# Performance work log

Hardware: AMD Instinct MI355X
Metric: run time of the kernel (lower is better)

Reference implementation:

```python
import jax, jax.numpy as jnp
import numpy as np

EMBED = 1024
HEADS = 16
HEAD_DIM = EMBED // HEADS


def setup_inputs() -> dict:
    key = jax.random.key(0)
    ks = jax.random.split(key, 7)
    B, S = 4, 2048
    q = jax.random.normal(ks[0], (B, S, EMBED), dtype=jnp.float32)
    k = jax.random.normal(ks[1], (B, S, EMBED), dtype=jnp.float32)
    v = jax.random.normal(ks[2], (B, S, EMBED), dtype=jnp.float32)
    # causal mask, broadcast over heads: [B, 1, S, S]
    mask = jnp.broadcast_to(jnp.tril(jnp.ones((S, S), dtype=jnp.int32))[None, None], (B, 1, S, S))
    scale = 1.0 / np.sqrt(EMBED)
    w_q = jax.random.normal(ks[3], (EMBED, EMBED), dtype=jnp.float32) * scale
    w_k = jax.random.normal(ks[4], (EMBED, EMBED), dtype=jnp.float32) * scale
    w_v = jax.random.normal(ks[5], (EMBED, EMBED), dtype=jnp.float32) * scale
    w_o = jax.random.normal(ks[6], (EMBED, EMBED), dtype=jnp.float32) * scale
    return {"q": q, "k": k, "v": v, "mask": mask,
            "w_q": w_q, "w_k": w_k, "w_v": w_v, "w_o": w_o}


def reference(q, k, v, mask, w_q, w_k, w_v, w_o):
    B, S, _ = q.shape
    # Linear projections (torch Linear: x @ W^T), split into heads: [B,H,S,D]
    def proj(x, w):
        return (x @ w.T).reshape(B, -1, HEADS, HEAD_DIM).transpose(0, 2, 1, 3)
    qh, kh, vh = proj(q, w_q), proj(k, w_k), proj(v, w_v)
    scores = jnp.einsum('bhqd,bhkd->bhqk', qh, kh) / jnp.sqrt(jnp.float32(HEAD_DIM))
    scores = jnp.where(mask == 0, jnp.float32(-1e9), scores)
    attn = jax.nn.softmax(scores, axis=-1)
    # dropout is identity in eval/reference mode
    x = jnp.einsum('bhqk,bhkd->bhqd', attn, vh)  # [B,H,S,D]
    x = x.transpose(0, 2, 1, 3).reshape(B, S, HEADS * HEAD_DIM)
    return x @ w_o.T
```

## Files before the change

### kernel.cpp

```cpp
#include <hip/hip_runtime.h>

typedef unsigned short u16;
typedef __attribute__((ext_vector_type(8))) short v8s;
typedef __attribute__((ext_vector_type(4))) float v4f;

#define S_LEN  2048
#define NHEADS 16
#define DHEAD  64
#define EMB    1024

#if __has_builtin(__builtin_amdgcn_exp2f)
#define EXP2F __builtin_amdgcn_exp2f
#else
#define EXP2F exp2f
#endif

__device__ __forceinline__ u16 f32_bf16(float f) {
  union { float f; unsigned u; } x; x.f = f;
  unsigned r = x.u + 0x7fffu + ((x.u >> 16) & 1u);
  return (u16)(r >> 16);
}

__device__ __forceinline__ void async16(const void* g, void* l) {
  __builtin_amdgcn_global_load_lds(
      (const __attribute__((address_space(1))) unsigned int*)g,
      (__attribute__((address_space(3))) unsigned int*)l, 16, 0, 0);
}

__global__ __launch_bounds__(256) void cvt_all(
    const float4* __restrict__ s0, const float4* __restrict__ s1,
    const float4* __restrict__ s2, const float4* __restrict__ s3,
    const float4* __restrict__ s4, const float4* __restrict__ s5,
    const float4* __restrict__ s6,
    ushort4* __restrict__ d0, ushort4* __restrict__ d1,
    ushort4* __restrict__ d2, ushort4* __restrict__ d3,
    ushort4* __restrict__ d4, ushort4* __restrict__ d5,
    ushort4* __restrict__ d6, int nbig, int nsmall) {
  const int y = blockIdx.y;
  const float4* s; ushort4* d;
  switch (y) {
    case 0: s = s0; d = d0; break;  case 1: s = s1; d = d1; break;
    case 2: s = s2; d = d2; break;  case 3: s = s3; d = d3; break;
    case 4: s = s4; d = d4; break;  case 5: s = s5; d = d5; break;
    default: s = s6; d = d6; break;
  }
  const int n4 = (y < 3) ? nbig : nsmall;
  for (int i = blockIdx.x * 256 + threadIdx.x; i < n4; i += gridDim.x * 256) {
    const float4 v = s[i];
    ushort4 o;
    o.x = f32_bf16(v.x); o.y = f32_bf16(v.y);
    o.z = f32_bf16(v.z); o.w = f32_bf16(v.w);
    d[i] = o;
  }
}

template <int MODE>
__global__ __launch_bounds__(512, 2) void gemm2ph(
    const u16* __restrict__ A, const u16* __restrict__ W0,
    const u16* __restrict__ W1, const u16* __restrict__ W2,
    u16* __restrict__ Cq, u16* __restrict__ Ck, u16* __restrict__ Cv,
    float* __restrict__ Cf, int mtiles) {
  const int K = 1024;
  const int NKT = 16;
  __shared__ __align__(16) u16 lA[2][128 * 64];
  __shared__ __align__(16) u16 lB[2][128 * 64];
  const int t = threadIdx.x;
  const int lane = t & 63, wv = t >> 6;
  const int wm = wv >> 2, wn = wv & 3;
  const int qr = lane >> 4, cl = lane & 15;

  const int nwg = gridDim.x;
  const int sid = (blockIdx.x & 7) * (nwg >> 3) + (blockIdx.x >> 3);
  const int bm = sid % mtiles, bn = sid / mtiles;
  const int m0 = bm << 7, n0 = bn << 7;
  const int sec = (MODE == 0) ? (m0 >> 13) : 0;
  const u16* W =
      (MODE == 0) ? ((sec == 0) ? W0 : (sec == 1) ? W1 : W2) : W0;

  v4f acc[4][2];
#pragma unroll
  for (int i = 0; i < 4; ++i)
#pragma unroll
    for (int j = 0; j < 2; ++j) acc[i][j] = (v4f){0.f, 0.f, 0.f, 0.f};

  const int srow = t >> 3;
  const int sw = ((t & 7) ^ (srow & 7)) << 3;
  const u16* aS[2];
  const u16* bS[2];
#pragma unroll
  for (int u = 0; u < 2; ++u) {
    aS[u] = A + (size_t)(m0 + srow + u * 64) * K + sw;
    bS[u] = W + (size_t)(n0 + srow + u * 64) * K + sw;
  }

#pragma unroll
  for (int u = 0; u < 2; ++u) async16(aS[u], &lA[0][(t + (u << 9)) << 3]);
#pragma unroll
  for (int u = 0; u < 2; ++u) async16(bS[u], &lB[0][(t + (u << 9)) << 3]);
  __syncthreads();

  for (int kt = 0; kt < NKT; ++kt) {
    const int cur = kt & 1;
    if (kt + 1 < NKT) {
      const int off = (kt + 1) << 6;
#pragma unroll
      for (int u = 0; u < 2; ++u)
        async16(aS[u] + off, &lA[1 - cur][(t + (u << 9)) << 3]);
#pragma unroll
      for (int u = 0; u < 2; ++u)
        async16(bS[u] + off, &lB[1 - cur][(t + (u << 9)) << 3]);
    }
    v8s a[4][2], b[2][2];
#pragma unroll
    for (int mf = 0; mf < 4; ++mf)
#pragma unroll
      for (int kh = 0; kh < 2; ++kh) {
        const int R = wm * 64 + mf * 16 + cl;
        a[mf][kh] =
            *(const v8s*)&lA[cur][R * 64 + ((((kh << 2) + qr) ^ (R & 7)) << 3)];
      }
#pragma unroll
    for (int nf = 0; nf < 2; ++nf)
#pragma unroll
      for (int kh = 0; kh < 2; ++kh) {
        const int R = wn * 32 + nf * 16 + cl;
        b[nf][kh] =
            *(const v8s*)&lB[cur][R * 64 + ((((kh << 2) + qr) ^ (R & 7)) << 3)];
      }
    __builtin_amdgcn_s_setprio(1);
#pragma unroll
    for (int kh = 0; kh < 2; ++kh)
#pragma unroll
      for (int mf = 0; mf < 4; ++mf)
#pragma unroll
        for (int nf = 0; nf < 2; ++nf)
          acc[mf][nf] = __builtin_amdgcn_mfma_f32_16x16x32_bf16(
              a[mf][kh], b[nf][kh], acc[mf][nf], 0, 0, 0);
    __builtin_amdgcn_s_setprio(0);
    __syncthreads();
  }

  if constexpr (MODE == 0) {
    u16* C = (sec == 0) ? Cq : (sec == 1) ? Ck : Cv;
#pragma unroll
    for (int mf = 0; mf < 4; ++mf)
#pragma unroll
      for (int nf = 0; nf < 2; ++nf)
#pragma unroll
        for (int r = 0; r < 4; ++r) {
          const int mloc = (m0 & 8191) + wm * 64 + mf * 16 + qr * 4 + r;
          const int n = n0 + wn * 32 + nf * 16 + cl;
          const int bb = mloc >> 11, s = mloc & (S_LEN - 1);
          const int h = n >> 6, d = n & (DHEAD - 1);
          const size_t idx =
              (sec < 2) ? (((size_t)bb * NHEADS + h) * S_LEN + s) * DHEAD + d
                        : (((size_t)bb * NHEADS + h) * DHEAD + d) * S_LEN + s;
          C[idx] = f32_bf16(acc[mf][nf][r]);
        }
  } else {
#pragma unroll
    for (int mf = 0; mf < 4; ++mf)
#pragma unroll
      for (int nf = 0; nf < 2; ++nf)
#pragma unroll
        for (int r = 0; r < 4; ++r) {
          const int m = m0 + wm * 64 + mf * 16 + qr * 4 + r;
          const int n = n0 + wn * 32 + nf * 16 + cl;
          Cf[(size_t)m * 1024 + n] = acc[mf][nf][r];
        }
  }
}

__global__ __launch_bounds__(256, 2) void attn_causal(
    const u16* __restrict__ Qp, const u16* __restrict__ Kp,
    const u16* __restrict__ VpT, u16* __restrict__ Out) {
  __shared__ __align__(16) u16 lK[2][2][64 * 64];
  __shared__ __align__(16) u16 lV[2][2][64 * 64];
  __shared__ __align__(16) u16 pb[4][32 * 64];
  const int t = threadIdx.x;
  const int lane = t & 63, w = t >> 6;
  const int qr = lane >> 4, cl = lane & 15;
  const int id = blockIdx.x;
  const int col = (id & 7) + ((id >> 6) << 3);
  const int pair = (id >> 3) & 7;
  const int h = col & 15, b = col >> 4;
  const size_t bh = ((size_t)b * NHEADS + h) * S_LEN * DHEAD;
  const u16* Qb = Qp + bh;
  const u16* Kb = Kp + bh;
  const u16* Vb = VpT + bh;

  v8s vone;
#pragma unroll
  for (int j = 0; j < 8; ++j) vone[j] = (short)0x3F80;
  const float SC = 0.125f * 1.4426950408889634f;

#define STAGE_T(TILE, GP, SL)                                                 \
  do {                                                                        \
    const int kn_ = (TILE) << 6;                                              \
    _Pragma("unroll") for (int i_ = 0; i_ < 2; ++i_) {                        \
      const int c_ = t + (i_ << 8);                                           \
      const int krow_ = c_ >> 3, kdc_ = (c_ & 7) ^ (krow_ & 7);               \
      async16(Kb + (size_t)(kn_ + krow_) * DHEAD + kdc_ * 8,                  \
              &lK[GP][SL][(w * 64 + (i_ << 8)) * 8]);                         \
      const int vd_ = c_ >> 3, vkc_ = (c_ & 7) ^ (vd_ & 7);                   \
      async16(Vb + (size_t)vd_ * S_LEN + kn_ + vkc_ * 8,                      \
              &lV[GP][SL][(w * 64 + (i_ << 8)) * 8]);                         \
    }                                                                         \
  } while (0)

  for (int phase = 0; phase < 2; ++phase) {
    const int qt = phase == 0 ? (15 - pair) : pair;
    const int q0 = qt << 7;
    const int wr0 = q0 + w * 32;

    v8s aq[2][2];
#pragma unroll
    for (int mf = 0; mf < 2; ++mf)
#pragma unroll
      for (int kf = 0; kf < 2; ++kf)
        aq[mf][kf] = *(const v8s*)(Qb + (size_t)(wr0 + mf * 16 + cl) * DHEAD +
                                   kf * 32 + qr * 8);

    v4f o[2][4], lac[2];
#pragma unroll
    for (int mf = 0; mf < 2; ++mf) {
      lac[mf] = (v4f){0.f, 0.f, 0.f, 0.f};
#pragma unroll
      for (int nf = 0; nf < 4; ++nf) o[mf][nf] = (v4f){0.f, 0.f, 0.f, 0.f};
    }

    const int ngrp = qt + 1;
    __syncthreads();
    STAGE_T(0, 0, 0);
    STAGE_T(1, 0, 1);

    for (int g = 0; g < ngrp; ++g) {
      const int gp = g & 1;
      __syncthreads();
      if (g + 1 < ngrp) {
        STAGE_T(2 * g + 2, 1 - gp, 0);
        STAGE_T(2 * g + 3, 1 - gp, 1);
      }
#pragma unroll
      for (int sl = 0; sl < 2; ++sl) {
        const int kt = 2 * g + sl;
        const int k0 = kt << 6;
        if (k0 > wr0 + 31) continue;
        const u16* lKc = &lK[gp][sl][0];
        const u16* lVc = &lV[gp][sl][0];

        v4f sacc[2][4];
#pragma unroll
        for (int mf = 0; mf < 2; ++mf)
#pragma unroll
          for (int ni = 0; ni < 4; ++ni) sacc[mf][ni] = (v4f){0.f, 0.f, 0.f, 0.f};
#pragma unroll
        for (int kf = 0; kf < 2; ++kf)
#pragma unroll
          for (int ni = 0; ni < 4; ++ni) {
            const v8s bk = *(const v8s*)&lKc[((ni * 16 + cl) * 8 +
                                             (((kf << 2) + qr) ^ (cl & 7))) * 8];
            sacc[0][ni] = __builtin_amdgcn_mfma_f32_16x16x32_bf16(
                aq[0][kf], bk, sacc[0][ni], 0, 0, 0);
            sacc[1][ni] = __builtin_amdgcn_mfma_f32_16x16x32_bf16(
                aq[1][kf], bk, sacc[1][ni], 0, 0, 0);
          }

#pragma unroll
        for (int mf = 0; mf < 2; ++mf) {
          const int rowb0 = wr0 + mf * 16;
          if (k0 + 63 <= rowb0) {
#pragma unroll
            for (int ni = 0; ni < 4; ++ni) {
              const int kc = ni * 2 + (cl >> 3);
#pragma unroll
              for (int r = 0; r < 4; ++r) {
                const float e = EXP2F(sacc[mf][ni][r] * SC);
                pb[w][((kc * 32 + mf * 16 + r * 4 + qr) << 3) + (cl & 7)] =
                    (u16)(__float_as_uint(e) >> 16);
              }
            }
          } else {
            const int rowb = rowb0 + qr * 4;
#pragma unroll
            for (int ni = 0; ni < 4; ++ni) {
              const int colk = k0 + ni * 16 + cl;
              const int kc = ni * 2 + (cl >> 3);
#pragma unroll
              for (int r = 0; r < 4; ++r) {
                float e = EXP2F(sacc[mf][ni][r] * SC);
                if (colk > rowb + r) e = 0.f;
                pb[w][((kc * 32 + mf * 16 + r * 4 + qr) << 3) + (cl & 7)] =
                    (u16)(__float_as_uint(e) >> 16);
              }
            }
          }
        }

#pragma unroll
        for (int kf = 0; kf < 2; ++kf) {
          const int kc = (kf << 2) + qr;
          const int sig0 = ((cl & 3) << 2) + (cl >> 2);
          const v8s ap0 = *(const v8s*)&pb[w][((kc * 32 + sig0) << 3)];
          const v8s ap1 = *(const v8s*)&pb[w][((kc * 32 + 16 + sig0) << 3)];
          lac[0] = __builtin_amdgcn_mfma_f32_16x16x32_bf16(ap0, vone, lac[0], 0, 0, 0);
          lac[1] = __builtin_amdgcn_mfma_f32_16x16x32_bf16(ap1, vone, lac[1], 0, 0, 0);
#pragma unroll
          for (int nf = 0; nf < 4; ++nf) {
            const v8s bv = *(const v8s*)&lVc[((nf * 16 + cl) * 8 +
                                             (kc ^ (cl & 7))) * 8];
            o[0][nf] = __builtin_amdgcn_mfma_f32_16x16x32_bf16(ap0, bv, o[0][nf], 0, 0, 0);
            o[1][nf] = __builtin_amdgcn_mfma_f32_16x16x32_bf16(ap1, bv, o[1][nf], 0, 0, 0);
          }
        }
      }
    }

#pragma unroll
    for (int mf = 0; mf < 2; ++mf) {
      float inv[4];
#pragma unroll
      for (int r = 0; r < 4; ++r) inv[r] = 1.0f / lac[mf][r];
#pragma unroll
      for (int nf = 0; nf < 4; ++nf)
#pragma unroll
        for (int r = 0; r < 4; ++r) {
          const int row = wr0 + mf * 16 + qr * 4 + r;
          const int colo = h * DHEAD + nf * 16 + cl;
          Out[((size_t)b * S_LEN + row) * EMB + colo] = f32_bf16(o[mf][nf][r] * inv[r]);
        }
    }
  }
#undef STAGE_T
}

extern "C" void kernel_launch(void* const* d_in, const int* in_sizes, int n_in,
                              void* d_out, int out_size, void* d_ws, size_t ws_size,
                              hipStream_t stream) {
  (void)in_sizes; (void)n_in; (void)out_size; (void)ws_size;
  const float* q  = (const float*)d_in[0];
  const float* k  = (const float*)d_in[1];
  const float* v  = (const float*)d_in[2];
  const float* wq = (const float*)d_in[4];
  const float* wk = (const float*)d_in[5];
  const float* wv = (const float*)d_in[6];
  const float* wo = (const float*)d_in[7];
  float* out = (float*)d_out;

  const size_t MT = (size_t)4 * S_LEN * EMB;
  const size_t WT = (size_t)EMB * EMB;
  u16* p = (u16*)d_ws;
  u16* xq = p; p += MT;
  u16* xk = p; p += MT;
  u16* xv = p; p += MT;
  u16* wqb = p; p += WT;
  u16* wkb = p; p += WT;
  u16* wvb = p; p += WT;
  u16* wob = p; p += WT;
  u16* Qp = p; p += MT;
  u16* Kp = p; p += MT;
  u16* Vp = p; p += MT;
  u16* Ao = xq;

  const dim3 blk(256);
  hipLaunchKernelGGL(cvt_all, dim3(512, 7), blk, 0, stream,
                     (const float4*)q, (const float4*)k, (const float4*)v,
                     (const float4*)wq, (const float4*)wk, (const float4*)wv,
                     (const float4*)wo,
                     (ushort4*)xq, (ushort4*)xk, (ushort4*)xv,
                     (ushort4*)wqb, (ushort4*)wkb, (ushort4*)wvb, (ushort4*)wob,
                     (int)(MT / 4), (int)(WT / 4));
  hipLaunchKernelGGL((gemm2ph<0>), dim3(1536), dim3(512), 0, stream,
                     xq, wqb, wkb, wvb, Qp, Kp, Vp, (float*)nullptr, 192);
  hipLaunchKernelGGL(attn_causal, dim3(512), blk, 0, stream, Qp, Kp, Vp, Ao);
  hipLaunchKernelGGL((gemm2ph<1>), dim3(512), dim3(512), 0, stream,
                     Ao, wob, (const u16*)nullptr, (const u16*)nullptr,
                     (u16*)nullptr, (u16*)nullptr, (u16*)nullptr, out, 64);
}
```

Measured before the change: 340.7 us.

## Use triple-buffered K=32 LDS pipeline with vmcnt waits in projection GEMMs

The projection GEMMs move from a double-buffered K=64 tile loop to a three-stage ring of K=32 tiles. Each stage is prefetched two tiles ahead, and the per-iteration __syncthreads is replaced by an explicit s_waitcnt vmcnt plus a single barrier. LDS offsets are precomputed once under a new swizzle layout. The aim is to keep more global-to-LDS loads in flight so the MFMAs stall less on memory, at the cost of twice as many iterations and barriers and reliance on hand-managed wait counts.

```diff
diff --git a/kernel.cpp b/kernel.cpp
--- a/kernel.cpp
+++ b/kernel.cpp
@@ -26,6 +26,8 @@
       (const __attribute__((address_space(1))) unsigned int*)g,
       (__attribute__((address_space(3))) unsigned int*)l, 16, 0, 0);
 }
+
+#define FENCE() asm volatile("" ::: "memory")
 
 __global__ __launch_bounds__(256) void cvt_all(
     const float4* __restrict__ s0, const float4* __restrict__ s1,
@@ -55,15 +57,15 @@
 }
 
 template <int MODE>
-__global__ __launch_bounds__(512, 2) void gemm2ph(
+__global__ __launch_bounds__(512, 2) void gemm3p(
     const u16* __restrict__ A, const u16* __restrict__ W0,
     const u16* __restrict__ W1, const u16* __restrict__ W2,
     u16* __restrict__ Cq, u16* __restrict__ Ck, u16* __restrict__ Cv,
     float* __restrict__ Cf, int mtiles) {
   const int K = 1024;
-  const int NKT = 16;
-  __shared__ __align__(16) u16 lA[2][128 * 64];
-  __shared__ __align__(16) u16 lB[2][128 * 64];
+  const int NKT = 32;
+  __shared__ __align__(16) u16 lA[3][4096];
+  __shared__ __align__(16) u16 lB[3][4096];
   const int t = threadIdx.x;
   const int lane = t & 63, wv = t >> 6;
   const int wm = wv >> 2, wn = wv & 3;
@@ -83,62 +85,69 @@
 #pragma unroll
     for (int j = 0; j < 2; ++j) acc[i][j] = (v4f){0.f, 0.f, 0.f, 0.f};
 
-  const int srow = t >> 3;
-  const int sw = ((t & 7) ^ (srow & 7)) << 3;
-  const u16* aS[2];
-  const u16* bS[2];
-#pragma unroll
-  for (int u = 0; u < 2; ++u) {
-    aS[u] = A + (size_t)(m0 + srow + u * 64) * K + sw;
-    bS[u] = W + (size_t)(n0 + srow + u * 64) * K + sw;
-  }
-
-#pragma unroll
-  for (int u = 0; u < 2; ++u) async16(aS[u], &lA[0][(t + (u << 9)) << 3]);
-#pragma unroll
-  for (int u = 0; u < 2; ++u) async16(bS[u], &lB[0][(t + (u << 9)) << 3]);
-  __syncthreads();
-
+  const int Lt = t >> 3;
+  const int pt = (t & 7) ^ (Lt & 7);
+  const int rh = (pt >> 2) << 6;
+  const int kc8 = (pt & 3) << 3;
+  const u16* aS = A + (size_t)(m0 + Lt + rh) * K + kc8;
+  const u16* bS = W + (size_t)(n0 + Lt + rh) * K + kc8;
+
+  int aOff[4], bOff[2];
+#pragma unroll
+  for (int f = 0; f < 4; ++f) {
+    const int R = wm * 64 + f * 16 + cl;
+    aOff[f] = (R & 63) * 64 + (((((R >> 6) << 2) | qr) ^ (cl & 7)) << 3);
+  }
+#pragma unroll
+  for (int nf = 0; nf < 2; ++nf) {
+    const int R = wn * 32 + nf * 16 + cl;
+    bOff[nf] = (R & 63) * 64 + (((((R >> 6) << 2) | qr) ^ (cl & 7)) << 3);
+  }
+
+#define STG(TILE, BUF)                                                        \
+  do {                                                                        \
+    const int ko_ = (TILE) << 5;                                              \
+    async16(aS + ko_, &lA[BUF][t * 8]);                                       \
+    async16(bS + ko_, &lB[BUF][t * 8]);                                       \
+  } while (0)
+
+#define BODY(CUR)                                                             \
+  do {                                                                        \
+    v8s a_[4], b_[2];                                                         \
+    _Pragma("unroll") for (int mf = 0; mf < 4; ++mf)                          \
+        a_[mf] = *(const v8s*)&lA[CUR][aOff[mf]];                             \
+    _Pragma("unroll") for (int nf = 0; nf < 2; ++nf)                          \
+        b_[nf] = *(const v8s*)&lB[CUR][bOff[nf]];                             \
+    __builtin_amdgcn_s_setprio(1);                                            \
+    _Pragma("unroll") for (int mf = 0; mf < 4; ++mf)                          \
+        _Pragma("unroll") for (int nf = 0; nf < 2; ++nf)                      \
+            acc[mf][nf] = __builtin_amdgcn_mfma_f32_16x16x32_bf16(            \
+                a_[mf], b_[nf], acc[mf][nf], 0, 0, 0);                        \
+    __builtin_amdgcn_s_setprio(0);                                            \
+  } while (0)
+
+  STG(0, 0);
+  STG(1, 1);
+  FENCE();
+
+  int cur = 0, stg = 2;
   for (int kt = 0; kt < NKT; ++kt) {
-    const int cur = kt & 1;
-    if (kt + 1 < NKT) {
-      const int off = (kt + 1) << 6;
-#pragma unroll
-      for (int u = 0; u < 2; ++u)
-        async16(aS[u] + off, &lA[1 - cur][(t + (u << 9)) << 3]);
-#pragma unroll
-      for (int u = 0; u < 2; ++u)
-        async16(bS[u] + off, &lB[1 - cur][(t + (u << 9)) << 3]);
+    if (kt < NKT - 1) {
+      asm volatile("s_waitcnt vmcnt(2)" ::: "memory");
+    } else {
+      asm volatile("s_waitcnt vmcnt(0)" ::: "memory");
     }
-    v8s a[4][2], b[2][2];
-#pragma unroll
-    for (int mf = 0; mf < 4; ++mf)
-#pragma unroll
-      for (int kh = 0; kh < 2; ++kh) {
-        const int R = wm * 64 + mf * 16 + cl;
-        a[mf][kh] =
-            *(const v8s*)&lA[cur][R * 64 + ((((kh << 2) + qr) ^ (R & 7)) << 3)];
-      }
-#pragma unroll
-    for (int nf = 0; nf < 2; ++nf)
-#pragma unroll
-      for (int kh = 0; kh < 2; ++kh) {
-        const int R = wn * 32 + nf * 16 + cl;
-        b[nf][kh] =
-            *(const v8s*)&lB[cur][R * 64 + ((((kh << 2) + qr) ^ (R & 7)) << 3)];
-      }
-    __builtin_amdgcn_s_setprio(1);
-#pragma unroll
-    for (int kh = 0; kh < 2; ++kh)
-#pragma unroll
-      for (int mf = 0; mf < 4; ++mf)
-#pragma unroll
-        for (int nf = 0; nf < 2; ++nf)
-          acc[mf][nf] = __builtin_amdgcn_mfma_f32_16x16x32_bf16(
-              a[mf][kh], b[nf][kh], acc[mf][nf], 0, 0, 0);
-    __builtin_amdgcn_s_setprio(0);
-    __syncthreads();
-  }
+    FENCE();
+    __builtin_amdgcn_s_barrier();
+    FENCE();
+    if (kt + 2 < NKT) STG(kt + 2, stg);
+    BODY(cur);
+    cur = (cur == 2) ? 0 : cur + 1;
+    stg = (stg == 2) ? 0 : stg + 1;
+  }
+
+#undef STG
+#undef BODY
 
   if constexpr (MODE == 0) {
     u16* C = (sec == 0) ? Cq : (sec == 1) ? Ck : Cv;
@@ -370,10 +379,10 @@
                      (ushort4*)xq, (ushort4*)xk, (ushort4*)xv,
                      (ushort4*)wqb, (ushort4*)wkb, (ushort4*)wvb, (ushort4*)wob,
                      (int)(MT / 4), (int)(WT / 4));
-  hipLaunchKernelGGL((gemm2ph<0>), dim3(1536), dim3(512), 0, stream,
+  hipLaunchKernelGGL((gemm3p<0>), dim3(1536), dim3(512), 0, stream,
                      xq, wqb, wkb, wvb, Qp, Kp, Vp, (float*)nullptr, 192);
   hipLaunchKernelGGL(attn_causal, dim3(512), blk, 0, stream, Qp, Kp, Vp, Ao);
-  hipLaunchKernelGGL((gemm2ph<1>), dim3(512), dim3(512), 0, stream,
+  hipLaunchKernelGGL((gemm3p<1>), dim3(512), dim3(512), 0, stream,
                      Ao, wob, (const u16*)nullptr, (const u16*)nullptr,
                      (u16*)nullptr, (u16*)nullptr, (u16*)nullptr, out, 64);
 }
```

Result: slower. 353.0 us (+3.6%).

## Run both causal query tiles concurrently in one 512-thread attention block

Applied to the files above, without the earlier changes.

The attention kernel now processes the two paired query tiles (15-pair and pair) at the same time with 8 waves instead of sequentially with 4. The shared K/V tiles are staged once per key tile and reused by both halves, and staging changes from 2-tile groups to single-tile double buffering. This removes the second pass's redundant K/V loads and the serial phase, at the cost of larger blocks, more LDS for the probability buffers, and idle waves for the short tile once its causal range ends.

```diff
diff --git a/kernel.cpp b/kernel.cpp
--- a/kernel.cpp
+++ b/kernel.cpp
@@ -171,12 +171,12 @@
   }
 }
 
-__global__ __launch_bounds__(256, 2) void attn_causal(
+__global__ __launch_bounds__(512, 2) void attn_causal(
     const u16* __restrict__ Qp, const u16* __restrict__ Kp,
     const u16* __restrict__ VpT, u16* __restrict__ Out) {
-  __shared__ __align__(16) u16 lK[2][2][64 * 64];
-  __shared__ __align__(16) u16 lV[2][2][64 * 64];
-  __shared__ __align__(16) u16 pb[4][32 * 64];
+  __shared__ __align__(16) u16 lK[2][64 * 64];
+  __shared__ __align__(16) u16 lV[2][64 * 64];
+  __shared__ __align__(16) u16 pb[8][32 * 64];
   const int t = threadIdx.x;
   const int lane = t & 63, w = t >> 6;
   const int qr = lane >> 4, cl = lane & 15;
@@ -194,142 +194,123 @@
   for (int j = 0; j < 8; ++j) vone[j] = (short)0x3F80;
   const float SC = 0.125f * 1.4426950408889634f;
 
-#define STAGE_T(TILE, GP, SL)                                                 \
+#define STAGE_T(TILE, SL)                                                     \
   do {                                                                        \
     const int kn_ = (TILE) << 6;                                              \
-    _Pragma("unroll") for (int i_ = 0; i_ < 2; ++i_) {                        \
-      const int c_ = t + (i_ << 8);                                           \
-      const int krow_ = c_ >> 3, kdc_ = (c_ & 7) ^ (krow_ & 7);               \
-      async16(Kb + (size_t)(kn_ + krow_) * DHEAD + kdc_ * 8,                  \
-              &lK[GP][SL][(w * 64 + (i_ << 8)) * 8]);                         \
-      const int vd_ = c_ >> 3, vkc_ = (c_ & 7) ^ (vd_ & 7);                   \
-      async16(Vb + (size_t)vd_ * S_LEN + kn_ + vkc_ * 8,                      \
-              &lV[GP][SL][(w * 64 + (i_ << 8)) * 8]);                         \
-    }                                                                         \
+    const int r_ = t >> 3, c_ = (t & 7) ^ (r_ & 7);                           \
+    async16(Kb + (size_t)(kn_ + r_) * DHEAD + c_ * 8, &lK[SL][t * 8]);        \
+    async16(Vb + (size_t)r_ * S_LEN + kn_ + c_ * 8, &lV[SL][t * 8]);          \
   } while (0)
 
-  for (int phase = 0; phase < 2; ++phase) {
-    const int qt = phase == 0 ? (15 - pair) : pair;
-    const int q0 = qt << 7;
-    const int wr0 = q0 + w * 32;
-
-    v8s aq[2][2];
+  const int qt = (w < 4) ? (15 - pair) : pair;
+  const int q0 = qt << 7;
+  const int wr0 = q0 + (w & 3) * 32;
+  const int nkt = 32 - 2 * pair;
+
+  v8s aq[2][2];
+#pragma unroll
+  for (int mf = 0; mf < 2; ++mf)
+#pragma unroll
+    for (int kf = 0; kf < 2; ++kf)
+      aq[mf][kf] = *(const v8s*)(Qb + (size_t)(wr0 + mf * 16 + cl) * DHEAD +
+                                 kf * 32 + qr * 8);
+
+  v4f o[2][4], lac[2];
+#pragma unroll
+  for (int mf = 0; mf < 2; ++mf) {
+    lac[mf] = (v4f){0.f, 0.f, 0.f, 0.f};
+#pragma unroll
+    for (int nf = 0; nf < 4; ++nf) o[mf][nf] = (v4f){0.f, 0.f, 0.f, 0.f};
+  }
+
+  STAGE_T(0, 0);
+
+  for (int kt = 0; kt < nkt; ++kt) {
+    const int k0 = kt << 6;
+    const int cb = kt & 1;
+    __syncthreads();
+    if (kt + 1 < nkt) STAGE_T(kt + 1, 1 - cb);
+    if (k0 > wr0 + 31) continue;
+
+    v4f sacc[2][4];
 #pragma unroll
     for (int mf = 0; mf < 2; ++mf)
 #pragma unroll
-      for (int kf = 0; kf < 2; ++kf)
-        aq[mf][kf] = *(const v8s*)(Qb + (size_t)(wr0 + mf * 16 + cl) * DHEAD +
-                                   kf * 32 + qr * 8);
-
-    v4f o[2][4], lac[2];
+      for (int ni = 0; ni < 4; ++ni) sacc[mf][ni] = (v4f){0.f, 0.f, 0.f, 0.f};
+#pragma unroll
+    for (int kf = 0; kf < 2; ++kf)
+#pragma unroll
+      for (int ni = 0; ni < 4; ++ni) {
+        const v8s bk = *(const v8s*)&lK[cb][((ni * 16 + cl) * 8 +
+                                            (((kf << 2) + qr) ^ (cl & 7))) * 8];
+        sacc[0][ni] = __builtin_amdgcn_mfma_f32_16x16x32_bf16(aq[0][kf], bk,
+                                                              sacc[0][ni], 0, 0, 0);
+        sacc[1][ni] = __builtin_amdgcn_mfma_f32_16x16x32_bf16(aq[1][kf], bk,
+                                                              sacc[1][ni], 0, 0, 0);
+      }
+
 #pragma unroll
     for (int mf = 0; mf < 2; ++mf) {
-      lac[mf] = (v4f){0.f, 0.f, 0.f, 0.f};
-#pragma unroll
-      for (int nf = 0; nf < 4; ++nf) o[mf][nf] = (v4f){0.f, 0.f, 0.f, 0.f};
-    }
-
-    const int ngrp = qt + 1;
-    __syncthreads();
-    STAGE_T(0, 0, 0);
-    STAGE_T(1, 0, 1);
-
-    for (int g = 0; g < ngrp; ++g) {
-      const int gp = g & 1;
-      __syncthreads();
-      if (g + 1 < ngrp) {
-        STAGE_T(2 * g + 2, 1 - gp, 0);
-        STAGE_T(2 * g + 3, 1 - gp, 1);
-      }
-#pragma unroll
-      for (int sl = 0; sl < 2; ++sl) {
-        const int kt = 2 * g + sl;
-        const int k0 = kt << 6;
-        if (k0 > wr0 + 31) continue;
-        const u16* lKc = &lK[gp][sl][0];
-        const u16* lVc = &lV[gp][sl][0];
-
-        v4f sacc[2][4];
-#pragma unroll
-        for (int mf = 0; mf < 2; ++mf)
-#pragma unroll
-          for (int ni = 0; ni < 4; ++ni) sacc[mf][ni] = (v4f){0.f, 0.f, 0.f, 0.f};
-#pragma unroll
-        for (int kf = 0; kf < 2; ++kf)
-#pragma unroll
-          for (int ni = 0; ni < 4; ++ni) {
-            const v8s bk = *(const v8s*)&lKc[((ni * 16 + cl) * 8 +
-                                             (((kf << 2) + qr) ^ (cl & 7))) * 8];
-            sacc[0][ni] = __builtin_amdgcn_mfma_f32_16x16x32_bf16(
-                aq[0][kf], bk, sacc[0][ni], 0, 0, 0);
-            sacc[1][ni] = __builtin_amdgcn_mfma_f32_16x16x32_bf16(
-                aq[1][kf], bk, sacc[1][ni], 0, 0, 0);
-          }
-
-#pragma unroll
-        for (int mf = 0; mf < 2; ++mf) {
-          const int rowb0 = wr0 + mf * 16;
-          if (k0 + 63 <= rowb0) {
-#pragma unroll
-            for (int ni = 0; ni < 4; ++ni) {
-              const int kc = ni * 2 + (cl >> 3);
-#pragma unroll
-              for (int r = 0; r < 4; ++r) {
-                const float e = EXP2F(sacc[mf][ni][r] * SC);
-                pb[w][((kc * 32 + mf * 16 + r * 4 + qr) << 3) + (cl & 7)] =
-                    (u16)(__float_as_uint(e) >> 16);
-              }
-            }
-          } else {
-            const int rowb = rowb0 + qr * 4;
-#pragma unroll
-            for (int ni = 0; ni < 4; ++ni) {
-              const int colk = k0 + ni * 16 + cl;
-              const int kc = ni * 2 + (cl >> 3);
-#pragma unroll
-              for (int r = 0; r < 4; ++r) {
-                float e = EXP2F(sacc[mf][ni][r] * SC);
-                if (colk > rowb + r) e = 0.f;
-                pb[w][((kc * 32 + mf * 16 + r * 4 + qr) << 3) + (cl & 7)] =
-                    (u16)(__float_as_uint(e) >> 16);
-              }
-            }
+      const int rowb0 = wr0 + mf * 16;
+      if (k0 + 63 <= rowb0) {
+#pragma unroll
+        for (int ni = 0; ni < 4; ++ni) {
+          const int kc = ni * 2 + (cl >> 3);
+#pragma unroll
+          for (int r = 0; r < 4; ++r) {
+            const float e = EXP2F(sacc[mf][ni][r] * SC);
+            pb[w][((kc * 32 + mf * 16 + r * 4 + qr) << 3) + (cl & 7)] =
+                (u16)(__float_as_uint(e) >> 16);
           }
         }
-
-#pragma unroll
-        for (int kf = 0; kf < 2; ++kf) {
-          const int kc = (kf << 2) + qr;
-          const int sig0 = ((cl & 3) << 2) + (cl >> 2);
-          const v8s ap0 = *(const v8s*)&pb[w][((kc * 32 + sig0) << 3)];
-          const v8s ap1 = *(const v8s*)&pb[w][((kc * 32 + 16 + sig0) << 3)];
-          lac[0] = __builtin_amdgcn_mfma_f32_16x16x32_bf16(ap0, vone, lac[0], 0, 0, 0);
-          lac[1] = __builtin_amdgcn_mfma_f32_16x16x32_bf16(ap1, vone, lac[1], 0, 0, 0);
-#pragma unroll
-          for (int nf = 0; nf < 4; ++nf) {
-            const v8s bv = *(const v8s*)&lVc[((nf * 16 + cl) * 8 +
-                                             (kc ^ (cl & 7))) * 8];
-            o[0][nf] = __builtin_amdgcn_mfma_f32_16x16x32_bf16(ap0, bv, o[0][nf], 0, 0, 0);
-            o[1][nf] = __builtin_amdgcn_mfma_f32_16x16x32_bf16(ap1, bv, o[1][nf], 0, 0, 0);
+      } else {
+        const int rowb = rowb0 + qr * 4;
+#pragma unroll
+        for (int ni = 0; ni < 4; ++ni) {
+          const int colk = k0 + ni * 16 + cl;
+          const int kc = ni * 2 + (cl >> 3);
+#pragma unroll
+          for (int r = 0; r < 4; ++r) {
+            float e = EXP2F(sacc[mf][ni][r] * SC);
+            if (colk > rowb + r) e = 0.f;
+            pb[w][((kc * 32 + mf * 16 + r * 4 + qr) << 3) + (cl & 7)] =
+                (u16)(__float_as_uint(e) >> 16);
           }
         }
       }
     }
 
 #pragma unroll
-    for (int mf = 0; mf < 2; ++mf) {
-      float inv[4];
-#pragma unroll
-      for (int r = 0; r < 4; ++r) inv[r] = 1.0f / lac[mf][r];
-#pragma unroll
-      for (int nf = 0; nf < 4; ++nf)
-#pragma unroll
-        for (int r = 0; r < 4; ++r) {
-          const int row = wr0 + mf * 16 + qr * 4 + r;
-          const int colo = h * DHEAD + nf * 16 + cl;
-          Out[((size_t)b * S_LEN + row) * EMB + colo] = f32_bf16(o[mf][nf][r] * inv[r]);
-        }
+    for (int kf = 0; kf < 2; ++kf) {
+      const int kc = (kf << 2) + qr;
+      const int sig0 = ((cl & 3) << 2) + (cl >> 2);
+      const v8s ap0 = *(const v8s*)&pb[w][((kc * 32 + sig0) << 3)];
+      const v8s ap1 = *(const v8s*)&pb[w][((kc * 32 + 16 + sig0) << 3)];
+      lac[0] = __builtin_amdgcn_mfma_f32_16x16x32_bf16(ap0, vone, lac[0], 0, 0, 0);
+      lac[1] = __builtin_amdgcn_mfma_f32_16x16x32_bf16(ap1, vone, lac[1], 0, 0, 0);
+#pragma unroll
+      for (int nf = 0; nf < 4; ++nf) {
+        const v8s bv = *(const v8s*)&lV[cb][((nf * 16 + cl) * 8 +
+                                            (kc ^ (cl & 7))) * 8];
+        o[0][nf] = __builtin_amdgcn_mfma_f32_16x16x32_bf16(ap0, bv, o[0][nf], 0, 0, 0);
+        o[1][nf] = __builtin_amdgcn_mfma_f32_16x16x32_bf16(ap1, bv, o[1][nf], 0, 0, 0);
+      }
     }
+  }
+
+#pragma unroll
+  for (int mf = 0; mf < 2; ++mf) {
+    float inv[4];
+#pragma unroll
+    for (int r = 0; r < 4; ++r) inv[r] = 1.0f / lac[mf][r];
+#pragma unroll
+    for (int nf = 0; nf < 4; ++nf)
+#pragma unroll
+      for (int r = 0; r < 4; ++r) {
+        const int row = wr0 + mf * 16 + qr * 4 + r;
+        const int colo = h * DHEAD + nf * 16 + cl;
+        Out[((size_t)b * S_LEN + row) * EMB + colo] = f32_bf16(o[mf][nf][r] * inv[r]);
+      }
   }
 #undef STAGE_T
 }
@@ -372,7 +353,8 @@
                      (int)(MT / 4), (int)(WT / 4));
   hipLaunchKernelGGL((gemm2ph<0>), dim3(1536), dim3(512), 0, stream,
                      xq, wqb, wkb, wvb, Qp, Kp, Vp, (float*)nullptr, 192);
-  hipLaunchKernelGGL(attn_causal, dim3(512), blk, 0, stream, Qp, Kp, Vp, Ao);
+  hipLaunchKernelGGL(attn_causal, dim3(512), dim3(512), 0, stream,
+                     Qp, Kp, Vp, Ao);
   hipLaunchKernelGGL((gemm2ph<1>), dim3(512), dim3(512), 0, stream,
                      Ao, wob, (const u16*)nullptr, (const u16*)nullptr,
                      (u16*)nullptr, (u16*)nullptr, (u16*)nullptr, out, 64);
```

After: 375.6 us. 10.2% more time.

## Fuse fp32-to-bf16 activation conversion into the QKV projection GEMM

Applied to the files above, without the earlier changes.

The standalone conversion of the q/k/v activations to bf16 is removed. The QKV GEMM now loads fp32 rows directly into registers, converts them, and writes the bf16 values into swizzled LDS for the next k-tile after the MFMA block, replacing the async global-to-LDS path for the A operand. This drops a full write and re-read of the three bf16 activation buffers. In exchange, the GEMM reads twice as many bytes for A, uses more registers for the fp32 staging values, and does the conversion ALU work inside the main loop.

```diff
diff --git a/kernel.cpp b/kernel.cpp
--- a/kernel.cpp
+++ b/kernel.cpp
@@ -27,24 +27,17 @@
       (__attribute__((address_space(3))) unsigned int*)l, 16, 0, 0);
 }
 
-__global__ __launch_bounds__(256) void cvt_all(
+__global__ __launch_bounds__(256) void cvt_w(
     const float4* __restrict__ s0, const float4* __restrict__ s1,
     const float4* __restrict__ s2, const float4* __restrict__ s3,
-    const float4* __restrict__ s4, const float4* __restrict__ s5,
-    const float4* __restrict__ s6,
     ushort4* __restrict__ d0, ushort4* __restrict__ d1,
-    ushort4* __restrict__ d2, ushort4* __restrict__ d3,
-    ushort4* __restrict__ d4, ushort4* __restrict__ d5,
-    ushort4* __restrict__ d6, int nbig, int nsmall) {
+    ushort4* __restrict__ d2, ushort4* __restrict__ d3, int n4) {
   const int y = blockIdx.y;
   const float4* s; ushort4* d;
   switch (y) {
     case 0: s = s0; d = d0; break;  case 1: s = s1; d = d1; break;
-    case 2: s = s2; d = d2; break;  case 3: s = s3; d = d3; break;
-    case 4: s = s4; d = d4; break;  case 5: s = s5; d = d5; break;
-    default: s = s6; d = d6; break;
-  }
-  const int n4 = (y < 3) ? nbig : nsmall;
+    case 2: s = s2; d = d2; break;  default: s = s3; d = d3; break;
+  }
   for (int i = blockIdx.x * 256 + threadIdx.x; i < n4; i += gridDim.x * 256) {
     const float4 v = s[i];
     ushort4 o;
@@ -56,8 +49,11 @@
 
 template <int MODE>
 __global__ __launch_bounds__(512, 2) void gemm2ph(
-    const u16* __restrict__ A, const u16* __restrict__ W0,
-    const u16* __restrict__ W1, const u16* __restrict__ W2,
+    const float* __restrict__ F0, const float* __restrict__ F1,
+    const float* __restrict__ F2,
+    const u16* __restrict__ Abf,
+    const u16* __restrict__ W0, const u16* __restrict__ W1,
+    const u16* __restrict__ W2,
     u16* __restrict__ Cq, u16* __restrict__ Ck, u16* __restrict__ Cv,
     float* __restrict__ Cf, int mtiles) {
   const int K = 1024;
@@ -84,28 +80,67 @@
     for (int j = 0; j < 2; ++j) acc[i][j] = (v4f){0.f, 0.f, 0.f, 0.f};
 
   const int srow = t >> 3;
-  const int sw = ((t & 7) ^ (srow & 7)) << 3;
+  const int swe = ((t & 7) ^ (srow & 7)) << 3;
+
+  const float* fS[2];
   const u16* aS[2];
   const u16* bS[2];
-#pragma unroll
-  for (int u = 0; u < 2; ++u) {
-    aS[u] = A + (size_t)(m0 + srow + u * 64) * K + sw;
-    bS[u] = W + (size_t)(n0 + srow + u * 64) * K + sw;
-  }
-
-#pragma unroll
-  for (int u = 0; u < 2; ++u) async16(aS[u], &lA[0][(t + (u << 9)) << 3]);
+  if constexpr (MODE == 0) {
+    const int mloc = m0 & 8191;
+    const float* Fs = (sec == 0) ? F0 : (sec == 1) ? F1 : F2;
+#pragma unroll
+    for (int u = 0; u < 2; ++u)
+      fS[u] = Fs + (size_t)(mloc + srow + u * 64) * K + swe;
+  } else {
+#pragma unroll
+    for (int u = 0; u < 2; ++u)
+      aS[u] = Abf + (size_t)(m0 + srow + u * 64) * K + swe;
+  }
+#pragma unroll
+  for (int u = 0; u < 2; ++u)
+    bS[u] = W + (size_t)(n0 + srow + u * 64) * K + swe;
+
+#define CVT_WRITE(U, BUF, LO, HI)                                             \
+  do {                                                                        \
+    v8s pk_;                                                                  \
+    pk_[0] = (short)f32_bf16((LO).x); pk_[1] = (short)f32_bf16((LO).y);       \
+    pk_[2] = (short)f32_bf16((LO).z); pk_[3] = (short)f32_bf16((LO).w);       \
+    pk_[4] = (short)f32_bf16((HI).x); pk_[5] = (short)f32_bf16((HI).y);       \
+    pk_[6] = (short)f32_bf16((HI).z); pk_[7] = (short)f32_bf16((HI).w);       \
+    *(v8s*)&lA[BUF][(t + ((U) << 9)) << 3] = pk_;                             \
+  } while (0)
+
+  if constexpr (MODE == 0) {
+#pragma unroll
+    for (int u = 0; u < 2; ++u) {
+      const float4 lo = *(const float4*)(fS[u]);
+      const float4 hi = *(const float4*)(fS[u] + 4);
+      CVT_WRITE(u, 0, lo, hi);
+    }
+  } else {
+#pragma unroll
+    for (int u = 0; u < 2; ++u) async16(aS[u], &lA[0][(t + (u << 9)) << 3]);
+  }
 #pragma unroll
   for (int u = 0; u < 2; ++u) async16(bS[u], &lB[0][(t + (u << 9)) << 3]);
   __syncthreads();
 
   for (int kt = 0; kt < NKT; ++kt) {
     const int cur = kt & 1;
+    float4 fa0[2], fa1[2];
     if (kt + 1 < NKT) {
       const int off = (kt + 1) << 6;
-#pragma unroll
-      for (int u = 0; u < 2; ++u)
-        async16(aS[u] + off, &lA[1 - cur][(t + (u << 9)) << 3]);
+      if constexpr (MODE == 0) {
+#pragma unroll
+        for (int u = 0; u < 2; ++u) {
+          fa0[u] = *(const float4*)(fS[u] + off);
+          fa1[u] = *(const float4*)(fS[u] + off + 4);
+        }
+      } else {
+#pragma unroll
+        for (int u = 0; u < 2; ++u)
+          async16(aS[u] + off, &lA[1 - cur][(t + (u << 9)) << 3]);
+      }
 #pragma unroll
       for (int u = 0; u < 2; ++u)
         async16(bS[u] + off, &lB[1 - cur][(t + (u << 9)) << 3]);
@@ -137,8 +172,15 @@
           acc[mf][nf] = __builtin_amdgcn_mfma_f32_16x16x32_bf16(
               a[mf][kh], b[nf][kh], acc[mf][nf], 0, 0, 0);
     __builtin_amdgcn_s_setprio(0);
+    if constexpr (MODE == 0) {
+      if (kt + 1 < NKT) {
+#pragma unroll
+        for (int u = 0; u < 2; ++u) CVT_WRITE(u, 1 - cur, fa0[u], fa1[u]);
+      }
+    }
     __syncthreads();
   }
+#undef CVT_WRITE
 
   if constexpr (MODE == 0) {
     u16* C = (sec == 0) ? Cq : (sec == 1) ? Ck : Cv;
@@ -350,9 +392,6 @@
   const size_t MT = (size_t)4 * S_LEN * EMB;
   const size_t WT = (size_t)EMB * EMB;
   u16* p = (u16*)d_ws;
-  u16* xq = p; p += MT;
-  u16* xk = p; p += MT;
-  u16* xv = p; p += MT;
   u16* wqb = p; p += WT;
   u16* wkb = p; p += WT;
   u16* wvb = p; p += WT;
@@ -360,20 +399,21 @@
   u16* Qp = p; p += MT;
   u16* Kp = p; p += MT;
   u16* Vp = p; p += MT;
-  u16* Ao = xq;
-
-  const dim3 blk(256);
-  hipLaunchKernelGGL(cvt_all, dim3(512, 7), blk, 0, stream,
-                     (const float4*)q, (const float4*)k, (const float4*)v,
+  u16* Ao = p; p += MT;
+
+  hipLaunchKernelGGL(cvt_w, dim3(128, 4), dim3(256), 0, stream,
                      (const float4*)wq, (const float4*)wk, (const float4*)wv,
                      (const float4*)wo,
-                     (ushort4*)xq, (ushort4*)xk, (ushort4*)xv,
                      (ushort4*)wqb, (ushort4*)wkb, (ushort4*)wvb, (ushort4*)wob,
-                     (int)(MT / 4), (int)(WT / 4));
+                     (int)(WT / 4));
   hipLaunchKernelGGL((gemm2ph<0>), dim3(1536), dim3(512), 0, stream,
-                     xq, wqb, wkb, wvb, Qp, Kp, Vp, (float*)nullptr, 192);
-  hipLaunchKernelGGL(attn_causal, dim3(512), blk, 0, stream, Qp, Kp, Vp, Ao);
+                     q, k, v, (const u16*)nullptr,
+                     wqb, wkb, wvb, Qp, Kp, Vp, (float*)nullptr, 192);
+  hipLaunchKernelGGL(attn_causal, dim3(512), dim3(256), 0, stream,
+                     Qp, Kp, Vp, Ao);
   hipLaunchKernelGGL((gemm2ph<1>), dim3(512), dim3(512), 0, stream,
-                     Ao, wob, (const u16*)nullptr, (const u16*)nullptr,
+                     (const float*)nullptr, (const float*)nullptr,
+                     (const float*)nullptr, Ao,
+                     wob, (const u16*)nullptr, (const u16*)nullptr,
                      (u16*)nullptr, (u16*)nullptr, (u16*)nullptr, out, 64);
 }
```

New measurement: 361.0 us. 6.0% more time.
